# Kernel tuning notes

Hardware: AMD Instinct MI355X
Metric: run time of the kernel (lower is better)

## Reference

```python
import jax, jax.numpy as jnp
import numpy as np

KH = KW = 3
STRIDE = 1
PAD = 1
DIL = 1


def im2col(x, kh, kw, stride, pad, dil):
    """F.unfold equivalent: x (N,C,H,W) -> (N,C,kh,kw,oh,ow)."""
    n, c, h, w = x.shape
    oh = (h + 2 * pad - dil * (kh - 1) - 1) // stride + 1
    ow = (w + 2 * pad - dil * (kw - 1) - 1) // stride + 1
    xp = jnp.pad(x, ((0, 0), (0, 0), (pad, pad), (pad, pad)))
    rows = []
    for i in range(kh):
        cols = []
        for j in range(kw):
            patch = jax.lax.slice(
                xp,
                (0, 0, i * dil, j * dil),
                (n, c, i * dil + (oh - 1) * stride + 1, j * dil + (ow - 1) * stride + 1),
                (1, 1, stride, stride),
            )  # (N,C,oh,ow)
            cols.append(patch)
        rows.append(jnp.stack(cols, axis=2))  # (N,C,kw,oh,ow)
    return jnp.stack(rows, axis=2)  # (N,C,kh,kw,oh,ow)


def setup_inputs() -> dict:
    key = jax.random.key(0)
    k1, k2, k3, k4 = jax.random.split(key, 4)
    N, Cin, Cout, H, W = 4, 64, 64, 128, 128
    x = jax.random.normal(k1, (N, Cin, H, W), dtype=jnp.float32)
    # adapting kernel: positive values (softmax-like output in EdgeKernel2d)
    kernel = jax.random.uniform(k2, (N, 1, KH, KW, H, W), dtype=jnp.float32, minval=0.01, maxval=1.0)
    fan_in = Cin * KH * KW
    weight = jax.random.normal(k3, (Cout, Cin, KH, KW), dtype=jnp.float32) * (1.0 / np.sqrt(fan_in))
    bias = jax.random.normal(k4, (Cout,), dtype=jnp.float32) * 0.01
    return {"x": x, "kernel": kernel, "weight": weight, "bias": bias}


def reference(x, kernel, weight, bias):
    # im_cols: (N,Cin,kh,kw,oh,ow)
    im_cols = im2col(x, KH, KW, STRIDE, PAD, DIL)
    in_mul_k = im_cols * kernel  # kernel broadcasts over Cin
    # dominate = sum_{k,l} in_mul_k / sum_{k,l} kernel  -> (N,Cin,oh,ow)
    dominate = in_mul_k.sum(axis=(2, 3)) / kernel.sum(axis=(2, 3))
    corrected = in_mul_k + dominate[:, :, None, None] * (1.0 - kernel)
    out = jnp.einsum('ncklhw,ockl->nohw', corrected, weight)
    out = out + bias[None, :, None, None]
    return out
```

## Files before the change

kernel.cpp:

```cpp
#include <hip/hip_runtime.h>
#include <hip/hip_bf16.h>
#include <cstddef>

typedef __attribute__((ext_vector_type(8))) short bf16x8;
typedef __attribute__((ext_vector_type(4))) float f32x4;
typedef __attribute__((ext_vector_type(2))) unsigned int u32x2;

#define NB 4
#define CIN 64
#define COUT 64
#define HH 128
#define WW 128
#define TAPS 9
#define STRD 82

__device__ __forceinline__ unsigned short f2bf(float f) {
    union { float f; unsigned u; } v; v.f = f;
    unsigned u = v.u + 0x7FFFu + ((v.u >> 16) & 1u);
    return (unsigned short)(u >> 16);
}

__global__ void prep_weight(const float* __restrict__ w, unsigned short* __restrict__ wBv) {
    int idx = blockIdx.x * blockDim.x + threadIdx.x;
    if (idx >= 40960) return;
    int e    = idx & 7;
    int lane = (idx >> 3) & 63;
    int fid  = idx >> 9;
    int wv   = fid / 20;
    int rem  = fid - wv * 20;
    int chunk = rem / 5;
    int step  = rem - chunk * 5;
    int l15 = lane & 15, g = lane >> 4;
    int o  = wv * 16 + l15;
    int kk = step * 32 + g * 8 + e;
    unsigned short v = 0;
    if (kk < 144) {
        int tap = kk >> 4;
        int cl  = kk & 15;
        v = f2bf(w[(o * CIN + chunk * 16 + cl) * TAPS + tap]);
    }
    wBv[idx] = v;
}

__launch_bounds__(256, 8)
__global__ void pac_conv(const float* __restrict__ x, const float* __restrict__ Kp,
                         const unsigned short* __restrict__ wBv,
                         const float* __restrict__ bias,
                         float* __restrict__ out) {
    __shared__ unsigned int sCor[32][STRD];

    const int blk0 = blockIdx.x;
    const int blk  = ((blk0 & 7) << 8) | (blk0 >> 3);

    const int w0 = (blk & 3) * 32;
    const int h  = (blk >> 2) & (HH - 1);
    const int n  = blk >> 9;

    const int t    = threadIdx.x;
    const int lane = t & 63;
    const int wv   = __builtin_amdgcn_readfirstlane(t >> 6);
    const int px   = lane & 31;
    const int cpair = t >> 5;

    float kreg[TAPS];
    float ks = 0.f;
    const float* kp = Kp + ((size_t)n * TAPS * HH + h) * WW + w0 + px;
    #pragma unroll
    for (int tap = 0; tap < TAPS; ++tap) {
        kreg[tap] = kp[(size_t)tap * HH * WW];
        ks += kreg[tap];
    }
    const float inv = 1.0f / ks;

    sCor[t >> 3][72 + (t & 7)] = 0u;

    const bool mL = (w0 == 0)  && (px == 0);
    const bool mR = (w0 == 96) && (px == 31);
    const unsigned voffL = (mL ? 1u : (unsigned)px) * 4u;
    const unsigned voffC = ((unsigned)px + 1u) * 4u;
    const unsigned voffR = (mR ? (unsigned)px : (unsigned)px + 2u) * 4u;

    const int l15 = lane & 15;
    const int g   = lane >> 4;
    const float bval = bias[wv * 16 + l15];

    f32x4 acc[2];
    acc[0] = (f32x4){0.f, 0.f, 0.f, 0.f};
    acc[1] = (f32x4){0.f, 0.f, 0.f, 0.f};

    #pragma unroll
    for (int chunk = 0; chunk < 4; ++chunk) {
        const int c0 = chunk * 16 + cpair * 2;
        const float* xb = x + (size_t)(n * CIN + c0) * (HH * WW) + w0 - 1;

        unsigned int cor[TAPS];
        float cprev[TAPS];
        #pragma unroll
        for (int j = 0; j < 2; ++j) {
            float xv[TAPS];
            #pragma unroll
            for (int k = 0; k < 3; ++k) {
                const int hh2 = h + k - 1;
                const bool hok = (unsigned)hh2 < (unsigned)HH;
                const int hc = hok ? hh2 : (hh2 < 0 ? 0 : HH - 1);
                const float* p = xb + (size_t)j * (HH * WW) + (size_t)hc * WW;
                float vL = *(const float*)((const char*)p + voffL);
                float vC = *(const float*)((const char*)p + voffC);
                float vR = *(const float*)((const char*)p + voffR);
                xv[k * 3 + 0] = (hok && !mL) ? vL : 0.f;
                xv[k * 3 + 1] = hok ? vC : 0.f;
                xv[k * 3 + 2] = (hok && !mR) ? vR : 0.f;
            }
            float s = 0.f;
            #pragma unroll
            for (int tap = 0; tap < TAPS; ++tap) s = fmaf(xv[tap], kreg[tap], s);
            const float d = s * inv;
            if (j == 0) {
                #pragma unroll
                for (int tap = 0; tap < TAPS; ++tap)
                    cprev[tap] = fmaf(kreg[tap], xv[tap] - d, d);
            } else {
                #pragma unroll
                for (int tap = 0; tap < TAPS; ++tap) {
                    float cc = fmaf(kreg[tap], xv[tap] - d, d);
                    union { __hip_bfloat162 h2; unsigned int u; } pk;
                    pk.h2 = __float22bfloat162_rn(make_float2(cprev[tap], cc));
                    cor[tap] = pk.u;
                }
            }
        }

        if (chunk) __syncthreads();
        #pragma unroll
        for (int tap = 0; tap < TAPS; ++tap)
            sCor[px][tap * 8 + cpair] = cor[tap];
        __syncthreads();

        const unsigned short* wfb =
            wBv + (((size_t)(wv * 20 + chunk * 5) << 6) + lane) * 8;
        #pragma unroll
        for (int step = 0; step < 5; ++step) {
            bf16x8 bfrag = *reinterpret_cast<const bf16x8*>(wfb + (step << 9));
            #pragma unroll
            for (int pt = 0; pt < 2; ++pt) {
                const unsigned int* ap = &sCor[pt * 16 + l15][step * 16 + g * 4];
                u32x2 alo = *reinterpret_cast<const u32x2*>(ap);
                u32x2 ahi = *reinterpret_cast<const u32x2*>(ap + 2);
                union { u32x2 p[2]; bf16x8 f; } af;
                af.p[0] = alo; af.p[1] = ahi;
                acc[pt] = __builtin_amdgcn_mfma_f32_16x16x32_bf16(af.f, bfrag, acc[pt], 0, 0, 0);
            }
        }
    }

    const int o = wv * 16 + l15;
    float* op = out + (((size_t)n * COUT + o) * HH + h) * WW + w0 + g * 4;
    #pragma unroll
    for (int pt = 0; pt < 2; ++pt) {
        f32x4 v = acc[pt];
        #pragma unroll
        for (int r = 0; r < 4; ++r) v[r] += bval;
        *reinterpret_cast<f32x4*>(op + pt * 16) = v;
    }
}

extern "C" void kernel_launch(void* const* d_in, const int* in_sizes, int n_in,
                              void* d_out, int out_size, void* d_ws, size_t ws_size,
                              hipStream_t stream) {
    const float* x    = (const float*)d_in[0];
    const float* Kp   = (const float*)d_in[1];
    const float* wgt  = (const float*)d_in[2];
    const float* bias = (const float*)d_in[3];
    float* out = (float*)d_out;
    unsigned short* wBv = (unsigned short*)d_ws;

    prep_weight<<<160, 256, 0, stream>>>(wgt, wBv);

    pac_conv<<<NB * HH * (WW / 32), 256, 0, stream>>>(x, Kp, wBv, bias, out);
}
```

Measured before the change: 28.91 us.

## Drop weight prep kernel; read fp32 weights directly in natural channel-tap order

Removes the separate weight-repacking kernel launch and instead has each wave load fp32 weights straight from the original layout and convert them to bf16 in registers. To make this work, the K ordering of the shared-memory correction tile is changed from tap-major to channel-major (channel pair times 9 taps), which matches contiguous weight rows. This saves one launch and a workspace round trip, at the cost of redundant per-block weight loads and conversions, plus a relaxed launch bound that may change occupancy.

New measurement: 47.83 us. 65.4% more time.

```diff
diff --git a/kernel.cpp b/kernel.cpp
--- a/kernel.cpp
+++ b/kernel.cpp
@@ -14,37 +14,10 @@
 #define TAPS 9
 #define STRD 82
 
-__device__ __forceinline__ unsigned short f2bf(float f) {
-    union { float f; unsigned u; } v; v.f = f;
-    unsigned u = v.u + 0x7FFFu + ((v.u >> 16) & 1u);
-    return (unsigned short)(u >> 16);
-}
 
-__global__ void prep_weight(const float* __restrict__ w, unsigned short* __restrict__ wBv) {
-    int idx = blockIdx.x * blockDim.x + threadIdx.x;
-    if (idx >= 40960) return;
-    int e    = idx & 7;
-    int lane = (idx >> 3) & 63;
-    int fid  = idx >> 9;
-    int wv   = fid / 20;
-    int rem  = fid - wv * 20;
-    int chunk = rem / 5;
-    int step  = rem - chunk * 5;
-    int l15 = lane & 15, g = lane >> 4;
-    int o  = wv * 16 + l15;
-    int kk = step * 32 + g * 8 + e;
-    unsigned short v = 0;
-    if (kk < 144) {
-        int tap = kk >> 4;
-        int cl  = kk & 15;
-        v = f2bf(w[(o * CIN + chunk * 16 + cl) * TAPS + tap]);
-    }
-    wBv[idx] = v;
-}
-
-__launch_bounds__(256, 8)
+__launch_bounds__(256)
 __global__ void pac_conv(const float* __restrict__ x, const float* __restrict__ Kp,
-                         const unsigned short* __restrict__ wBv,
+                         const float* __restrict__ w,
                          const float* __restrict__ bias,
                          float* __restrict__ out) {
     __shared__ unsigned int sCor[32][STRD];
@@ -82,7 +55,9 @@
 
     const int l15 = lane & 15;
     const int g   = lane >> 4;
-    const float bval = bias[wv * 16 + l15];
+    const int o   = wv * 16 + l15;
+    const float bval = bias[o];
+    const float* wbase0 = w + (size_t)o * (CIN * TAPS) + g * 8;
 
     f32x4 acc[2];
     acc[0] = (f32x4){0.f, 0.f, 0.f, 0.f};
@@ -93,8 +68,7 @@
         const int c0 = chunk * 16 + cpair * 2;
         const float* xb = x + (size_t)(n * CIN + c0) * (HH * WW) + w0 - 1;
 
-        unsigned int cor[TAPS];
-        float cprev[TAPS];
+        float cch[2][TAPS];
         #pragma unroll
         for (int j = 0; j < 2; ++j) {
             float xv[TAPS];
@@ -115,32 +89,48 @@
             #pragma unroll
             for (int tap = 0; tap < TAPS; ++tap) s = fmaf(xv[tap], kreg[tap], s);
             const float d = s * inv;
-            if (j == 0) {
-                #pragma unroll
-                for (int tap = 0; tap < TAPS; ++tap)
-                    cprev[tap] = fmaf(kreg[tap], xv[tap] - d, d);
-            } else {
-                #pragma unroll
-                for (int tap = 0; tap < TAPS; ++tap) {
-                    float cc = fmaf(kreg[tap], xv[tap] - d, d);
-                    union { __hip_bfloat162 h2; unsigned int u; } pk;
-                    pk.h2 = __float22bfloat162_rn(make_float2(cprev[tap], cc));
-                    cor[tap] = pk.u;
-                }
-            }
+            #pragma unroll
+            for (int tap = 0; tap < TAPS; ++tap)
+                cch[j][tap] = fmaf(kreg[tap], xv[tap] - d, d);
+        }
+
+        unsigned int cor9[9];
+        #pragma unroll
+        for (int i = 0; i < 9; ++i) {
+            const int s0 = 2 * i, s1 = 2 * i + 1;
+            const float f0 = cch[s0 / 9][s0 % 9];
+            const float f1 = cch[s1 / 9][s1 % 9];
+            union { __hip_bfloat162 h2; unsigned int u; } pk;
+            pk.h2 = __float22bfloat162_rn(make_float2(f0, f1));
+            cor9[i] = pk.u;
         }
 
         if (chunk) __syncthreads();
         #pragma unroll
-        for (int tap = 0; tap < TAPS; ++tap)
-            sCor[px][tap * 8 + cpair] = cor[tap];
+        for (int i = 0; i < 9; ++i)
+            sCor[px][cpair * 9 + i] = cor9[i];
         __syncthreads();
 
-        const unsigned short* wfb =
-            wBv + (((size_t)(wv * 20 + chunk * 5) << 6) + lane) * 8;
+        const float* wc = wbase0 + chunk * 144;
         #pragma unroll
         for (int step = 0; step < 5; ++step) {
-            bf16x8 bfrag = *reinterpret_cast<const bf16x8*>(wfb + (step << 9));
+            bf16x8 bfrag;
+            if (step < 4 || g < 2) {
+                f32x4 wlo = *reinterpret_cast<const f32x4*>(wc + step * 32);
+                f32x4 whi = *reinterpret_cast<const f32x4*>(wc + step * 32 + 4);
+                union { unsigned int u[4]; bf16x8 f; } bp;
+                #pragma unroll
+                for (int i = 0; i < 2; ++i) {
+                    union { __hip_bfloat162 h2; unsigned int u; } a, b;
+                    a.h2 = __float22bfloat162_rn(make_float2(wlo[2 * i], wlo[2 * i + 1]));
+                    b.h2 = __float22bfloat162_rn(make_float2(whi[2 * i], whi[2 * i + 1]));
+                    bp.u[i] = a.u;
+                    bp.u[2 + i] = b.u;
+                }
+                bfrag = bp.f;
+            } else {
+                bfrag = (bf16x8){0, 0, 0, 0, 0, 0, 0, 0};
+            }
             #pragma unroll
             for (int pt = 0; pt < 2; ++pt) {
                 const unsigned int* ap = &sCor[pt * 16 + l15][step * 16 + g * 4];
@@ -153,7 +143,6 @@
         }
     }
 
-    const int o = wv * 16 + l15;
     float* op = out + (((size_t)n * COUT + o) * HH + h) * WW + w0 + g * 4;
     #pragma unroll
     for (int pt = 0; pt < 2; ++pt) {
@@ -172,9 +161,6 @@
     const float* wgt  = (const float*)d_in[2];
     const float* bias = (const float*)d_in[3];
     float* out = (float*)d_out;
-    unsigned short* wBv = (unsigned short*)d_ws;
 
-    prep_weight<<<160, 256, 0, stream>>>(wgt, wBv);
-
-    pac_conv<<<NB * HH * (WW / 32), 256, 0, stream>>>(x, Kp, wBv, bias, out);
+    pac_conv<<<NB * HH * (WW / 32), 256, 0, stream>>>(x, Kp, wgt, bias, out);
 }
```

## Build MFMA A-fragments in registers, dropping LDS staging and barriers

Applied to the files above, without the earlier changes.

Each lane now computes the corrected values directly in the K-ordering the MFMA A operand expects (4 channels by 9 taps per lane group). The shared-memory transpose and the __syncthreads around it are gone, and the weight prep is reordered to match the new K layout. Blocks shrink to 16 pixels, so the grid doubles and x reads are repeated across the four waves of a block. Each wave now recomputes all corrections redundantly, which multiplies the scalar ALU and load work per pixel; padding also increases with 36 useful of 40 K slots.

Result: slower. 47.40 us (+64.0%).

```diff
diff --git a/kernel.cpp b/kernel.cpp
--- a/kernel.cpp
+++ b/kernel.cpp
@@ -4,7 +4,6 @@
 
 typedef __attribute__((ext_vector_type(8))) short bf16x8;
 typedef __attribute__((ext_vector_type(4))) float f32x4;
-typedef __attribute__((ext_vector_type(2))) unsigned int u32x2;
 
 #define NB 4
 #define CIN 64
@@ -12,7 +11,7 @@
 #define HH 128
 #define WW 128
 #define TAPS 9
-#define STRD 82
+#define HW (HH * WW)
 
 __device__ __forceinline__ unsigned short f2bf(float f) {
     union { float f; unsigned u; } v; v.f = f;
@@ -29,81 +28,79 @@
     int wv   = fid / 20;
     int rem  = fid - wv * 20;
     int chunk = rem / 5;
-    int step  = rem - chunk * 5;
+    int s     = rem - chunk * 5;
     int l15 = lane & 15, g = lane >> 4;
     int o  = wv * 16 + l15;
-    int kk = step * 32 + g * 8 + e;
+    int L  = s * 8 + e;
     unsigned short v = 0;
-    if (kk < 144) {
-        int tap = kk >> 4;
-        int cl  = kk & 15;
-        v = f2bf(w[(o * CIN + chunk * 16 + cl) * TAPS + tap]);
+    if (L < 36) {
+        int c   = chunk * 16 + 4 * g + L / 9;
+        int tap = L % 9;
+        v = f2bf(w[(o * CIN + c) * TAPS + tap]);
     }
     wBv[idx] = v;
 }
 
-__launch_bounds__(256, 8)
+__launch_bounds__(256)
 __global__ void pac_conv(const float* __restrict__ x, const float* __restrict__ Kp,
                          const unsigned short* __restrict__ wBv,
                          const float* __restrict__ bias,
                          float* __restrict__ out) {
-    __shared__ unsigned int sCor[32][STRD];
 
     const int blk0 = blockIdx.x;
-    const int blk  = ((blk0 & 7) << 8) | (blk0 >> 3);
+    const int blk  = ((blk0 & 7) << 9) | (blk0 >> 3);
 
-    const int w0 = (blk & 3) * 32;
-    const int h  = (blk >> 2) & (HH - 1);
-    const int n  = blk >> 9;
+    const int wt = blk & 7;
+    const int h  = (blk >> 3) & (HH - 1);
+    const int n  = blk >> 10;
+    const int w0 = wt * 16;
 
     const int t    = threadIdx.x;
     const int lane = t & 63;
     const int wv   = __builtin_amdgcn_readfirstlane(t >> 6);
-    const int px   = lane & 31;
-    const int cpair = t >> 5;
+    const int l15  = lane & 15;
+    const int g    = lane >> 4;
 
     float kreg[TAPS];
     float ks = 0.f;
-    const float* kp = Kp + ((size_t)n * TAPS * HH + h) * WW + w0 + px;
+    const float* kp = Kp + ((size_t)n * TAPS * HH + h) * WW + w0 + l15;
     #pragma unroll
     for (int tap = 0; tap < TAPS; ++tap) {
-        kreg[tap] = kp[(size_t)tap * HH * WW];
+        kreg[tap] = kp[(size_t)tap * HW];
         ks += kreg[tap];
     }
     const float inv = 1.0f / ks;
 
-    sCor[t >> 3][72 + (t & 7)] = 0u;
+    const bool mL = (w0 == 0)       && (l15 == 0);
+    const bool mR = (w0 == WW - 16) && (l15 == 15);
+    const unsigned voffL = (mL ? 1u : (unsigned)l15) * 4u;
+    const unsigned voffC = ((unsigned)l15 + 1u) * 4u;
+    const unsigned voffR = (mR ? (unsigned)l15 : (unsigned)l15 + 2u) * 4u;
 
-    const bool mL = (w0 == 0)  && (px == 0);
-    const bool mR = (w0 == 96) && (px == 31);
-    const unsigned voffL = (mL ? 1u : (unsigned)px) * 4u;
-    const unsigned voffC = ((unsigned)px + 1u) * 4u;
-    const unsigned voffR = (mR ? (unsigned)px : (unsigned)px + 2u) * 4u;
-
-    const int l15 = lane & 15;
-    const int g   = lane >> 4;
     const float bval = bias[wv * 16 + l15];
-
-    f32x4 acc[2];
-    acc[0] = (f32x4){0.f, 0.f, 0.f, 0.f};
-    acc[1] = (f32x4){0.f, 0.f, 0.f, 0.f};
+    f32x4 acc = (f32x4){0.f, 0.f, 0.f, 0.f};
 
     #pragma unroll
     for (int chunk = 0; chunk < 4; ++chunk) {
-        const int c0 = chunk * 16 + cpair * 2;
-        const float* xb = x + (size_t)(n * CIN + c0) * (HH * WW) + w0 - 1;
+        const unsigned short* wfb =
+            wBv + (((size_t)(wv * 20 + chunk * 5) << 6) + lane) * 8;
+        bf16x8 bfr[5];
+        #pragma unroll
+        for (int s = 0; s < 5; ++s)
+            bfr[s] = *reinterpret_cast<const bf16x8*>(wfb + (s << 9));
 
-        unsigned int cor[TAPS];
-        float cprev[TAPS];
+        float cch[4][TAPS];
         #pragma unroll
-        for (int j = 0; j < 2; ++j) {
+        for (int j = 0; j < 4; ++j) {
+            const int c = chunk * 16 + 4 * g + j;
+            const float* xb = x + (size_t)(n * CIN + c) * HW + w0 - 1;
             float xv[TAPS];
             #pragma unroll
             for (int k = 0; k < 3; ++k) {
                 const int hh2 = h + k - 1;
                 const bool hok = (unsigned)hh2 < (unsigned)HH;
                 const int hc = hok ? hh2 : (hh2 < 0 ? 0 : HH - 1);
-                const float* p = xb + (size_t)j * (HH * WW) + (size_t)hc * WW;
+                const float* p = xb + (size_t)hc * WW;
                 float vL = *(const float*)((const char*)p + voffL);
                 float vC = *(const float*)((const char*)p + voffC);
                 float vR = *(const float*)((const char*)p + voffR);
@@ -115,53 +112,39 @@
             #pragma unroll
             for (int tap = 0; tap < TAPS; ++tap) s = fmaf(xv[tap], kreg[tap], s);
             const float d = s * inv;
-            if (j == 0) {
-                #pragma unroll
-                for (int tap = 0; tap < TAPS; ++tap)
-                    cprev[tap] = fmaf(kreg[tap], xv[tap] - d, d);
-            } else {
-                #pragma unroll
-                for (int tap = 0; tap < TAPS; ++tap) {
-                    float cc = fmaf(kreg[tap], xv[tap] - d, d);
-                    union { __hip_bfloat162 h2; unsigned int u; } pk;
-                    pk.h2 = __float22bfloat162_rn(make_float2(cprev[tap], cc));
-                    cor[tap] = pk.u;
-                }
+            #pragma unroll
+            for (int tap = 0; tap < TAPS; ++tap)
+                cch[j][tap] = fmaf(kreg[tap], xv[tap] - d, d);
+        }
+
+        unsigned int fr[5][4];
+        #pragma unroll
+        for (int s = 0; s < 5; ++s) {
+            #pragma unroll
+            for (int i = 0; i < 4; ++i) {
+                const int L0 = s * 8 + 2 * i, L1 = L0 + 1;
+                const float f0 = (L0 < 36) ? cch[L0 / 9][L0 % 9] : 0.f;
+                const float f1 = (L1 < 36) ? cch[L1 / 9][L1 % 9] : 0.f;
+                union { __hip_bfloat162 h2; unsigned int u; } pk;
+                pk.h2 = __float22bfloat162_rn(make_float2(f0, f1));
+                fr[s][i] = pk.u;
             }
         }
 
-        if (chunk) __syncthreads();
         #pragma unroll
-        for (int tap = 0; tap < TAPS; ++tap)
-            sCor[px][tap * 8 + cpair] = cor[tap];
-        __syncthreads();
-
-        const unsigned short* wfb =
-            wBv + (((size_t)(wv * 20 + chunk * 5) << 6) + lane) * 8;
-        #pragma unroll
-        for (int step = 0; step < 5; ++step) {
-            bf16x8 bfrag = *reinterpret_cast<const bf16x8*>(wfb + (step << 9));
-            #pragma unroll
-            for (int pt = 0; pt < 2; ++pt) {
-                const unsigned int* ap = &sCor[pt * 16 + l15][step * 16 + g * 4];
-                u32x2 alo = *reinterpret_cast<const u32x2*>(ap);
-                u32x2 ahi = *reinterpret_cast<const u32x2*>(ap + 2);
-                union { u32x2 p[2]; bf16x8 f; } af;
-                af.p[0] = alo; af.p[1] = ahi;
-                acc[pt] = __builtin_amdgcn_mfma_f32_16x16x32_bf16(af.f, bfrag, acc[pt], 0, 0, 0);
-            }
+        for (int s = 0; s < 5; ++s) {
+            union { unsigned int u[4]; bf16x8 f; } af;
+            af.u[0] = fr[s][0]; af.u[1] = fr[s][1];
+            af.u[2] = fr[s][2]; af.u[3] = fr[s][3];
+            acc = __builtin_amdgcn_mfma_f32_16x16x32_bf16(af.f, bfr[s], acc, 0, 0, 0);
         }
     }
 
-    const int o = wv * 16 + l15;
-    float* op = out + (((size_t)n * COUT + o) * HH + h) * WW + w0 + g * 4;
+    float* op = out + (((size_t)n * COUT + wv * 16 + l15) * HH + h) * WW + w0 + g * 4;
+    f32x4 v = acc;
     #pragma unroll
-    for (int pt = 0; pt < 2; ++pt) {
-        f32x4 v = acc[pt];
-        #pragma unroll
-        for (int r = 0; r < 4; ++r) v[r] += bval;
-        *reinterpret_cast<f32x4*>(op + pt * 16) = v;
-    }
+    for (int r = 0; r < 4; ++r) v[r] += bval;
+    *reinterpret_cast<f32x4*>(op) = v;
 }
 
 extern "C" void kernel_launch(void* const* d_in, const int* in_sizes, int n_in,
@@ -176,5 +159,5 @@
 
     prep_weight<<<160, 256, 0, stream>>>(wgt, wBv);
 
-    pac_conv<<<NB * HH * (WW / 32), 256, 0, stream>>>(x, Kp, wBv, bias, out);
+    pac_conv<<<NB * HH * (WW / 16), 256, 0, stream>>>(x, Kp, wBv, bias, out);
 }
```
